# Optimization experiments

Hardware: AMD Instinct MI355X
Metric: run time of the kernel (lower is better)

## Reference

```python
import jax, jax.numpy as jnp
import numpy as np


def setup_inputs() -> dict:
    key = jax.random.key(0)
    k1, k2 = jax.random.split(key)
    x = jax.random.normal(k1, (4, 1, 16384), dtype=jnp.float32)  # [B, C, T]
    # dictionary initialized uniform(-1, 1) as in nn.Parameter(...).uniform_(-1, 1)
    d = jax.random.uniform(k2, (256, 1, 256), dtype=jnp.float32, minval=-1.0, maxval=1.0)  # [A, C, K]
    return {"x": x, "d": d, "n_iterations": 16}


def reference(x, d, n_iterations):
    B, C, T = x.shape
    A, _, K = d.shape
    pad = K // 2
    # normalize each atom over (channels, atom_size) dims, i.e. d_normalization_dims=(-1,-2)
    norms = jnp.linalg.norm(d.reshape(A, -1), axis=-1)
    dn = d / (norms[:, None, None] + 1e-12)

    # work in a padded domain so conv output position == start index in padded residual
    rp = jnp.pad(x, ((0, 0), (0, 0), (pad, pad)))        # residual, [B, C, T+2*pad]
    recon = jnp.zeros_like(rp)                            # accumulated reconstruction
    Tout = T + 2 * pad - K + 1                            # conv output length

    def step(carry, _):
        rp, recon = carry
        # cross-correlation of residual with every atom: [B, A, Tout]
        fm = jax.lax.conv_general_dilated(
            rp, dn, window_strides=(1,), padding='VALID',
            dimension_numbers=('NCH', 'OIH', 'NCH'))
        flat = fm.reshape(B, A * Tout)
        idx = jnp.argmax(flat, axis=-1)                   # signed max, per batch item
        val = jnp.take_along_axis(flat, idx[:, None], axis=-1)[:, 0]
        atom_idx = idx // Tout
        pos = idx % Tout                                  # start index in padded domain
        atoms = dn[atom_idx] * val[:, None, None]         # [B, C, K]

        def upd(r, rec, a, p):
            seg = jax.lax.dynamic_slice(r, (0, p), (C, K))
            r2 = jax.lax.dynamic_update_slice(r, seg - a, (0, p))
            segr = jax.lax.dynamic_slice(rec, (0, p), (C, K))
            rec2 = jax.lax.dynamic_update_slice(rec, segr + a, (0, p))
            return r2, rec2

        rp2, recon2 = jax.vmap(upd)(rp, recon, atoms, pos)
        return (rp2, recon2), None

    (rp, recon), _ = jax.lax.scan(step, (rp, recon), None, length=n_iterations)
    # crop padding -> reconstruction with same shape as x
    return recon[:, :, pad:pad + T]
```

## Files before the change

### kernel.cpp

```cpp
#include <hip/hip_runtime.h>
#include <math.h>

#define B    4
#define T    16384
#define A    256
#define K    256
#define PAD  128
#define TP   (T + 2*PAD)
#define TOUT (TP - K + 1)
#define ITERS 16
#define CHUNK 512
#define NCHUNK 33
#define NCP  36
#define TILE 2048
#define NTILE 9
#define NBLK 512
#define BPB2 128
#define HBASE 8192
#define RPSTORE 8448
#define RPN 8704
#define NGRP 8
#define SUBSTRIDE 32
#define BARSTRIDE (NGRP*SUBSTRIDE)
#define DLDS 40960

#define TAP(acc, s0,s1,s2,s3, dq) { acc = fmaf(s0,(dq).x,acc); acc = fmaf(s1,(dq).y,acc); \
                                    acc = fmaf(s2,(dq).z,acc); acc = fmaf(s3,(dq).w,acc); }

__device__ __forceinline__ void wave_amax(float& bv, int& bi) {
    #pragma unroll
    for (int off = 32; off; off >>= 1) {
        float ov = __shfl_down(bv, off);
        int   oi = __shfl_down(bi, off);
        if (ov > bv || (ov == bv && oi < bi)) { bv = ov; bi = oi; }
    }
}

struct KSmem {
    float  rp[RPN];
    float4 dn4[4][64];
    float  chv[4][34];
    int    chi[4][34];
    float  wv[16]; int wi[16];
    float  fv; int fi;
};

__device__ __forceinline__ void gbar_sub(unsigned* sub, int r, unsigned gen16, int tid,
                                         bool release_arrival, bool acquire_exit) {
    __syncthreads();
    if (tid == 0)
        __hip_atomic_fetch_add(&sub[(r >> 4)*SUBSTRIDE], 1u,
                               release_arrival ? __ATOMIC_RELEASE : __ATOMIC_RELAXED,
                               __HIP_MEMORY_SCOPE_AGENT);
    if (tid < 64) {
        for (;;) {
            unsigned ok = 1;
            if (tid < NGRP)
                ok = (__hip_atomic_load(&sub[tid*SUBSTRIDE], __ATOMIC_RELAXED,
                                        __HIP_MEMORY_SCOPE_AGENT) >= gen16);
            if (__all((int)ok)) break;
            __builtin_amdgcn_s_sleep(4);
        }
    }
    __syncthreads();
    if (acquire_exit) __builtin_amdgcn_fence(__ATOMIC_ACQUIRE, "agent");
}

__device__ void chunks_update(KSmem& sm, int baseF, int cA, int cB, int aBase, int tid) {
    const int lane = tid & 63, w = tid >> 6;
    const int grp = tid >> 7;
    const int cg = grp ? cB : cA;
    const int lt = cg*512 + (tid & 127)*4;
    float c0[4] = {0,0,0,0}, c1[4] = {0,0,0,0}, c2[4] = {0,0,0,0}, c3[4] = {0,0,0,0};
    if (cg >= 0) {
        const float4* srp4 = (const float4*)sm.rp;
        int ol4 = (lt - baseF) >> 2;
        float4 p = srp4[ol4];
        #pragma unroll 4
        for (int kq = 0; kq < 64; kq++) {
            float4 d0 = sm.dn4[0][kq];
            float4 d1 = sm.dn4[1][kq];
            float4 d2 = sm.dn4[2][kq];
            float4 d3 = sm.dn4[3][kq];
            float4 pn = srp4[ol4 + kq + 1];
            TAP(c0[0], p.x,p.y,p.z,p.w, d0); TAP(c0[1], p.y,p.z,p.w,pn.x, d0);
            TAP(c0[2], p.z,p.w,pn.x,pn.y, d0); TAP(c0[3], p.w,pn.x,pn.y,pn.z, d0);
            TAP(c1[0], p.x,p.y,p.z,p.w, d1); TAP(c1[1], p.y,p.z,p.w,pn.x, d1);
            TAP(c1[2], p.z,p.w,pn.x,pn.y, d1); TAP(c1[3], p.w,pn.x,pn.y,pn.z, d1);
            TAP(c2[0], p.x,p.y,p.z,p.w, d2); TAP(c2[1], p.y,p.z,p.w,pn.x, d2);
            TAP(c2[2], p.z,p.w,pn.x,pn.y, d2); TAP(c2[3], p.w,pn.x,pn.y,pn.z, d2);
            TAP(c3[0], p.x,p.y,p.z,p.w, d3); TAP(c3[1], p.y,p.z,p.w,pn.x, d3);
            TAP(c3[2], p.z,p.w,pn.x,pn.y, d3); TAP(c3[3], p.w,pn.x,pn.y,pn.z, d3);
            p = pn;
        }
    }
    float bv0 = -INFINITY, bv1 = -INFINITY, bv2 = -INFINITY, bv3 = -INFINITY;
    int bi0 = 0x7fffffff, bi1 = 0x7fffffff, bi2 = 0x7fffffff, bi3 = 0x7fffffff;
    if (cg >= 0) {
        #pragma unroll
        for (int j = 0; j < 4; j++) {
            int t = lt + j;
            if (t < TOUT) {
                if (c0[j] > bv0) { bv0 = c0[j]; bi0 = (aBase+0)*TOUT + t; }
                if (c1[j] > bv1) { bv1 = c1[j]; bi1 = (aBase+1)*TOUT + t; }
                if (c2[j] > bv2) { bv2 = c2[j]; bi2 = (aBase+2)*TOUT + t; }
                if (c3[j] > bv3) { bv3 = c3[j]; bi3 = (aBase+3)*TOUT + t; }
            }
        }
    }
    wave_amax(bv0, bi0); wave_amax(bv1, bi1); wave_amax(bv2, bi2); wave_amax(bv3, bi3);
    if (lane == 0) {
        sm.wv[0*4+w] = bv0; sm.wi[0*4+w] = bi0;
        sm.wv[1*4+w] = bv1; sm.wi[1*4+w] = bi1;
        sm.wv[2*4+w] = bv2; sm.wi[2*4+w] = bi2;
        sm.wv[3*4+w] = bv3; sm.wi[3*4+w] = bi3;
    }
    __syncthreads();
    if (tid < 8) {
        int a = tid >> 1, hh = tid & 1;
        int chunk = hh ? cB : cA;
        if (chunk >= 0) {
            float v0 = sm.wv[a*4 + 2*hh];   int i0 = sm.wi[a*4 + 2*hh];
            float v1 = sm.wv[a*4 + 2*hh+1]; int i1 = sm.wi[a*4 + 2*hh+1];
            if (v1 > v0 || (v1 == v0 && i1 < i0)) { v0 = v1; i0 = i1; }
            sm.chv[a][chunk] = v0; sm.chi[a][chunk] = i0;
        }
    }
    __syncthreads();
}

__device__ __forceinline__ void best_write1(KSmem& sm, int slot, int h, int tid,
                                            float* __restrict__ abv, int* __restrict__ abi) {
    const int lane = tid & 63, w = tid >> 6;
    int cstart = h ? 16 : 0, nch = h ? 17 : 16;
    float bv = -INFINITY; int bi = 0x7fffffff;
    if (lane < nch) { bv = sm.chv[w][cstart + lane]; bi = sm.chi[w][cstart + lane]; }
    wave_amax(bv, bi);
    if (lane == 0) { sm.wv[8+w] = bv; sm.wi[8+w] = bi; }
    __syncthreads();
    if (tid == 0) {
        float v = sm.wv[8]; int i = sm.wi[8];
        #pragma unroll
        for (int j = 1; j < 4; j++)
            if (sm.wv[8+j] > v || (sm.wv[8+j] == v && sm.wi[8+j] < i)) { v = sm.wv[8+j]; i = sm.wi[8+j]; }
        __hip_atomic_store(&abv[slot], v, __ATOMIC_RELAXED, __HIP_MEMORY_SCOPE_AGENT);
        __hip_atomic_store(&abi[slot], i, __ATOMIC_RELAXED, __HIP_MEMORY_SCOPE_AGENT);
    }
    asm volatile("s_waitcnt vmcnt(0)" ::: "memory");
}

__device__ __forceinline__ void pick1(KSmem& sm, int b, int tid,
                                      const float* __restrict__ avc, const int* __restrict__ aic) {
    const int lane = tid & 63, w = tid >> 6;
    float v = -INFINITY; int i = 0x7fffffff;
    if (tid < BPB2) {
        int s = b*BPB2 + tid;
        v = __hip_atomic_load(&avc[s], __ATOMIC_RELAXED, __HIP_MEMORY_SCOPE_AGENT);
        i = __hip_atomic_load(&aic[s], __ATOMIC_RELAXED, __HIP_MEMORY_SCOPE_AGENT);
    }
    if (w < 2) {
        wave_amax(v, i);
        if (lane == 0) { sm.wv[w] = v; sm.wi[w] = i; }
    }
    __syncthreads();
    if (tid == 0) {
        float bv = sm.wv[0]; int bi = sm.wi[0];
        if (sm.wv[1] > bv || (sm.wv[1] == bv && sm.wi[1] < bi)) { bv = sm.wv[1]; bi = sm.wi[1]; }
        sm.fv = bv; sm.fi = bi;
    }
    __syncthreads();
}

__global__ void __launch_bounds__(256, 2)
k_coop(const float* __restrict__ x, const float* __restrict__ d, float* __restrict__ out,
       float* __restrict__ dn,
       float* __restrict__ abv0, int* __restrict__ abi0,
       float* __restrict__ abv1, int* __restrict__ abi1, unsigned* __restrict__ bar) {
    extern __shared__ char raw[];
    KSmem& sm = *(KSmem*)raw;
    const int bid = blockIdx.x, tid = threadIdx.x;
    const int b = bid >> 7, r = bid & 127;
    const int h = r >> 6, a0 = r & 63;
    const int lane = tid & 63, w = tid >> 6;
    const int baseF = h * HBASE;
    const int cstart = h ? 16 : 0, cend = h ? 33 : 16;
    const int slot = b*BPB2 + r;
    unsigned* sub = bar + b*BARSTRIDE;

    {
        const float4* x4 = (const float4*)(x + (size_t)b*T);
        float4* rp4w = (float4*)sm.rp;
        int b4 = baseF >> 2;
        for (int i = tid; i < RPN/4; i += 256) {
            int g4 = b4 + i;
            float4 v = {0.f,0.f,0.f,0.f};
            if (i < RPSTORE/4 && g4 >= PAD/4 && g4 < (PAD+T)/4) v = x4[g4 - PAD/4];
            rp4w[i] = v;
        }
    }
    #pragma unroll
    for (int s = 0; s < 4; s++) {
        int atom = a0*4 + s;
        float v = d[atom*K + tid];
        float sq = v*v;
        #pragma unroll
        for (int off = 32; off; off >>= 1) sq += __shfl_down(sq, off);
        if (lane == 0) sm.wv[w] = sq;
        __syncthreads();
        float norm = sqrtf(sm.wv[0] + sm.wv[1] + sm.wv[2] + sm.wv[3]) + 1e-12f;
        float nv = v / norm;
        ((float*)&sm.dn4[s][0])[tid] = nv;
        dn[atom*K + tid] = nv;
        __syncthreads();
    }
    {
        int npass = h ? 9 : 8;
        for (int p = 0; p < npass; p++) {
            int ca = cstart + 2*p;
            int cb2 = (ca + 1 < cend) ? ca + 1 : -1;
            chunks_update(sm, baseF, ca, cb2, a0*4, tid);
        }
    }
    best_write1(sm, slot, h, tid, abv0, abi0);
    unsigned gen = 1;
    gbar_sub(sub, r, gen*16u, tid, true, true);

    const float* avc = abv0; const int* aic = abi0;
    float* avn = abv1; int* ain = abi1;
    for (int it = 0; it < ITERS-1; it++) {
        pick1(sm, b, tid, avc, aic);
        float val = sm.fv; int idx = sm.fi;
        int atom = idx / TOUT, pos = idx - atom*TOUT;
        float ds = dn[atom*K + tid];
        int li = pos + tid - baseF;
        if (li >= 0 && li < RPSTORE) sm.rp[li] -= val * ds;
        __syncthreads();
        int lo = pos - (K-1); if (lo < 0) lo = 0;
        int g0 = lo >> 9, g1 = g0 + 1;
        bool in0 = (g0 >= cstart && g0 < cend);
        bool in1 = (g1 >= cstart && g1 < cend);
        int ca = in0 ? g0 : (in1 ? g1 : -1);
        int cb2 = (in0 && in1) ? g1 : -1;
        if (ca >= 0) chunks_update(sm, baseF, ca, cb2, a0*4, tid);
        best_write1(sm, slot, h, tid, avn, ain);
        { const float* t1 = avc; avc = avn; avn = (float*)t1; }
        { const int*   t2 = aic; aic = ain; ain = (int*)t2; }
        gen++;
        gbar_sub(sub, r, gen*16u, tid, false, false);
    }
    if (a0 == 0) {
        pick1(sm, b, tid, avc, aic);
        float val = sm.fv; int idx = sm.fi;
        int atom = idx / TOUT, pos = idx - atom*TOUT;
        float ds = dn[atom*K + tid];
        int li = pos + tid - baseF;
        if (li >= 0 && li < RPSTORE) sm.rp[li] -= val * ds;
        __syncthreads();
        int o_lo4 = h ? (HBASE - PAD)/4 : 0;
        int o_hi4 = h ? T/4 : (HBASE - PAD)/4;
        const float4* xb4 = (const float4*)(x + (size_t)b*T);
        float4* o4 = (float4*)(out + (size_t)b*T);
        for (int i4 = o_lo4 + tid; i4 < o_hi4; i4 += 256) {
            float4 xv = xb4[i4];
            float4 rv = *(const float4*)&sm.rp[i4*4 + PAD - baseF];
            float4 ov; ov.x = xv.x - rv.x; ov.y = xv.y - rv.y;
            ov.z = xv.z - rv.z; ov.w = xv.w - rv.w;
            o4[i4] = ov;
        }
    }
}

struct Smem {
    float rp[TILE + K + 16];
    float dnA[K];
    float dnB[K];
    float dnsel[K];
    float wv[16]; int wi[16];
    float fv; int fi;
};

__device__ __forceinline__ void dev_norm(int a0, int tid, const float* __restrict__ d,
                                         float* __restrict__ dn, Smem& sm) {
    int lane = tid & 63, w = tid >> 6;
    #pragma unroll
    for (int s = 0; s < 2; s++) {
        int atom = a0*2 + s;
        float v = d[atom*K + tid];
        float sq = v*v;
        #pragma unroll
        for (int off = 32; off; off >>= 1) sq += __shfl_down(sq, off);
        if (lane == 0) sm.wv[w] = sq;
        __syncthreads();
        float norm = sqrtf(sm.wv[0] + sm.wv[1] + sm.wv[2] + sm.wv[3]) + 1e-12f;
        dn[atom*K + tid] = v / norm;
        __syncthreads();
    }
}

__device__ __forceinline__ void dev_init(int a0, int b, int tid, const float* __restrict__ x,
                                         float* __restrict__ rp, float* __restrict__ recon) {
    int i = a0*256 + tid;
    if (i < TP) {
        float v = (i >= PAD && i < PAD + T) ? x[b*T + (i - PAD)] : 0.f;
        rp[(size_t)b*TP + i] = v;
        recon[(size_t)b*TP + i] = 0.f;
    }
}

__device__ void dev_conv(int a0, int b, int tid, const float* __restrict__ rp,
                         const float* __restrict__ dn,
                         float* __restrict__ segval, int* __restrict__ segidx,
                         float* __restrict__ abv, int* __restrict__ abi, Smem& sm) {
    const int aA = a0*2, aB = a0*2 + 1;
    const int lane = tid & 63, w = tid >> 6;
    sm.dnA[tid] = dn[aA*K + tid];
    sm.dnB[tid] = dn[aB*K + tid];
    const float4* rp4 = (const float4*)(rp + (size_t)b*TP);

    for (int tile = 0; tile < NTILE; tile++) {
        int t0 = tile * TILE;
        __syncthreads();
        float4* s4 = (float4*)sm.rp;
        for (int i = tid; i < 580; i += 256) {
            int g = t0/4 + i;
            float4 v = {0.f,0.f,0.f,0.f};
            if (g*4 < TP) v = rp4[g];
            s4[i] = v;
        }
        __syncthreads();
        const float4* srp4 = (const float4*)sm.rp;
        const float4* dA4  = (const float4*)sm.dnA;
        const float4* dB4  = (const float4*)sm.dnB;
        float accA0[4] = {0,0,0,0}, accA1[4] = {0,0,0,0};
        float accB0[4] = {0,0,0,0}, accB1[4] = {0,0,0,0};
        float4 p = srp4[tid];
        float4 q = srp4[tid + 256];
        #pragma unroll 4
        for (int kq = 0; kq < 64; kq++) {
            float4 dA = dA4[kq];
            float4 dB = dB4[kq];
            float4 pn = srp4[tid + kq + 1];
            float4 qn = srp4[tid + 256 + kq + 1];
            TAP(accA0[0], p.x,p.y,p.z,p.w, dA); TAP(accA0[1], p.y,p.z,p.w,pn.x, dA);
            TAP(accA0[2], p.z,p.w,pn.x,pn.y, dA); TAP(accA0[3], p.w,pn.x,pn.y,pn.z, dA);
            TAP(accB0[0], p.x,p.y,p.z,p.w, dB); TAP(accB0[1], p.y,p.z,p.w,pn.x, dB);
            TAP(accB0[2], p.z,p.w,pn.x,pn.y, dB); TAP(accB0[3], p.w,pn.x,pn.y,pn.z, dB);
            TAP(accA1[0], q.x,q.y,q.z,q.w, dA); TAP(accA1[1], q.y,q.z,q.w,qn.x, dA);
            TAP(accA1[2], q.z,q.w,qn.x,qn.y, dA); TAP(accA1[3], q.w,qn.x,qn.y,qn.z, dA);
            TAP(accB1[0], q.x,q.y,q.z,q.w, dB); TAP(accB1[1], q.y,q.z,q.w,qn.x, dB);
            TAP(accB1[2], q.z,q.w,qn.x,qn.y, dB); TAP(accB1[3], q.w,qn.x,qn.y,qn.z, dB);
            p = pn; q = qn;
        }
        int lt = tid * 4;
        float bvA0 = -INFINITY, bvA1 = -INFINITY, bvB0 = -INFINITY, bvB1 = -INFINITY;
        int biA0 = 0x7fffffff, biA1 = 0x7fffffff, biB0 = 0x7fffffff, biB1 = 0x7fffffff;
        #pragma unroll
        for (int j = 0; j < 4; j++) {
            int t = t0 + lt + j;
            if (t < TOUT) {
                if (accA0[j] > bvA0) { bvA0 = accA0[j]; biA0 = aA*TOUT + t; }
                if (accB0[j] > bvB0) { bvB0 = accB0[j]; biB0 = aB*TOUT + t; }
            }
            int t1 = t0 + 1024 + lt + j;
            if (t1 < TOUT) {
                if (accA1[j] > bvA1) { bvA1 = accA1[j]; biA1 = aA*TOUT + t1; }
                if (accB1[j] > bvB1) { bvB1 = accB1[j]; biB1 = aB*TOUT + t1; }
            }
        }
        wave_amax(bvA0, biA0); wave_amax(bvA1, biA1);
        wave_amax(bvB0, biB0); wave_amax(bvB1, biB1);
        if (lane == 0) {
            sm.wv[w]    = bvA0; sm.wi[w]    = biA0;
            sm.wv[4+w]  = bvA1; sm.wi[4+w]  = biA1;
            sm.wv[8+w]  = bvB0; sm.wi[8+w]  = biB0;
            sm.wv[12+w] = bvB1; sm.wi[12+w] = biB1;
        }
        __syncthreads();
        if (tid < 4) {
            float v0 = sm.wv[2*tid];   int i0 = sm.wi[2*tid];
            float v1 = sm.wv[2*tid+1]; int i1 = sm.wi[2*tid+1];
            if (v1 > v0 || (v1 == v0 && i1 < i0)) { v0 = v1; i0 = i1; }
            int chunk = tile*4 + tid;
            if (chunk < NCHUNK) {
                segval[((size_t)b*A + aA)*NCP + chunk] = v0;
                segidx[((size_t)b*A + aA)*NCP + chunk] = i0;
            }
        } else if (tid >= 64 && tid < 68) {
            int c = tid - 64;
            float v0 = sm.wv[8+2*c];   int i0 = sm.wi[8+2*c];
            float v1 = sm.wv[8+2*c+1]; int i1 = sm.wi[8+2*c+1];
            if (v1 > v0 || (v1 == v0 && i1 < i0)) { v0 = v1; i0 = i1; }
            int chunk = tile*4 + c;
            if (chunk < NCHUNK) {
                segval[((size_t)b*A + aB)*NCP + chunk] = v0;
                segidx[((size_t)b*A + aB)*NCP + chunk] = i0;
            }
        }
    }
    __syncthreads();
    if (w < 2) {
        int atom = (w == 0) ? aA : aB;
        float bv = -INFINITY; int bi = 0x7fffffff;
        if (lane < NCHUNK) {
            bv = segval[((size_t)b*A + atom)*NCP + lane];
            bi = segidx[((size_t)b*A + atom)*NCP + lane];
        }
        wave_amax(bv, bi);
        if (lane == 0) { abv[b*A + atom] = bv; abi[b*A + atom] = bi; }
    }
}

__device__ void dev_iter(int a0, int b, int tid, int last,
                         const float* __restrict__ avc, const int* __restrict__ aic,
                         float* __restrict__ avn, int* __restrict__ ain,
                         const float* __restrict__ rin, float* __restrict__ rout,
                         float* __restrict__ recon, const float* __restrict__ dn,
                         float* __restrict__ segval, int* __restrict__ segidx, Smem& sm) {
    const int aA = a0*2, aB = a0*2 + 1;
    const int lane = tid & 63, w = tid >> 6;

    float bv0 = avc[b*A + tid]; int bi0 = aic[b*A + tid];
    const float4* rin4 = (const float4*)(rin + (size_t)b*TP);
    const int icopy = a0*256 + tid;
    const bool docopy = (!last) && (icopy < TP/4);
    float4 vcopy = {0.f,0.f,0.f,0.f};
    if (docopy) vcopy = rin4[icopy];
    sm.dnA[tid] = dn[aA*K + tid];
    sm.dnB[tid] = dn[aB*K + tid];

    {
        float bv = bv0; int bi = bi0;
        wave_amax(bv, bi);
        if (lane == 0) { sm.wv[w] = bv; sm.wi[w] = bi; }
        __syncthreads();
        if (tid == 0) {
            bv = sm.wv[0]; bi = sm.wi[0];
            for (int j = 1; j < 4; j++)
                if (sm.wv[j] > bv || (sm.wv[j] == bv && sm.wi[j] < bi)) { bv = sm.wv[j]; bi = sm.wi[j]; }
            sm.fv = bv; sm.fi = bi;
        }
        __syncthreads();
    }
    float val = sm.fv; int idx = sm.fi;
    int atom = idx / TOUT, pos = idx - atom*TOUT;
    sm.dnsel[tid] = dn[atom*K + tid];

    int lo = pos - (K-1); if (lo < 0) lo = 0;
    int c_lo = lo >> 9;
    int tbase = c_lo * CHUNK;

    if (!last) {
        float4* s4 = (float4*)sm.rp;
        for (int i = tid; i < 324; i += 256) {
            int g = tbase/4 + i;
            float4 v = {0.f,0.f,0.f,0.f};
            if (g*4 < TP) v = rin4[g];
            s4[i] = v;
        }
    }
    __syncthreads();
    if (docopy) {
        float4* rout4 = (float4*)(rout + (size_t)b*TP);
        float4 v = vcopy;
        int o = icopy*4 - pos;
        if (o > -4 && o < K) {
            if (o+0 >= 0 && o+0 < K) v.x -= val * sm.dnsel[o+0];
            if (o+1 >= 0 && o+1 < K) v.y -= val * sm.dnsel[o+1];
            if (o+2 >= 0 && o+2 < K) v.z -= val * sm.dnsel[o+2];
            if (o+3 >= 0 && o+3 < K) v.w -= val * sm.dnsel[o+3];
        }
        rout4[icopy] = v;
    }
    if (a0 == 0) {
        recon[(size_t)b*TP + pos + tid] += val * sm.dnsel[tid];
    }
    if (last) return;

    sm.rp[pos + tid - tbase] -= val * sm.dnsel[tid];
    __syncthreads();

    const float4* srp4 = (const float4*)sm.rp;
    const float4* dA4  = (const float4*)sm.dnA;
    const float4* dB4  = (const float4*)sm.dnB;
    float cA[4] = {0,0,0,0}, cB[4] = {0,0,0,0};
    float4 p = srp4[tid];
    #pragma unroll 4
    for (int kq = 0; kq < 64; kq++) {
        float4 dA = dA4[kq];
        float4 dB = dB4[kq];
        float4 pn = srp4[tid + kq + 1];
        TAP(cA[0], p.x,p.y,p.z,p.w, dA); TAP(cA[1], p.y,p.z,p.w,pn.x, dA);
        TAP(cA[2], p.z,p.w,pn.x,pn.y, dA); TAP(cA[3], p.w,pn.x,pn.y,pn.z, dA);
        TAP(cB[0], p.x,p.y,p.z,p.w, dB); TAP(cB[1], p.y,p.z,p.w,pn.x, dB);
        TAP(cB[2], p.z,p.w,pn.x,pn.y, dB); TAP(cB[3], p.w,pn.x,pn.y,pn.z, dB);
        p = pn;
    }
    int lt = tid * 4;
    float bvA = -INFINITY, bvB = -INFINITY;
    int biA = 0x7fffffff, biB = 0x7fffffff;
    #pragma unroll
    for (int j = 0; j < 4; j++) {
        int t = tbase + lt + j;
        if (t < TOUT) {
            if (cA[j] > bvA) { bvA = cA[j]; biA = aA*TOUT + t; }
            if (cB[j] > bvB) { bvB = cB[j]; biB = aB*TOUT + t; }
        }
    }
    wave_amax(bvA, biA); wave_amax(bvB, biB);
    if (lane == 0) { sm.wv[w] = bvA; sm.wi[w] = biA; sm.wv[8+w] = bvB; sm.wi[8+w] = biB; }
    __syncthreads();
    if (tid < 2) {
        float v0 = sm.wv[2*tid];   int i0 = sm.wi[2*tid];
        float v1 = sm.wv[2*tid+1]; int i1 = sm.wi[2*tid+1];
        if (v1 > v0 || (v1 == v0 && i1 < i0)) { v0 = v1; i0 = i1; }
        int chunk = c_lo + tid;
        if (chunk < NCHUNK) {
            segval[((size_t)b*A + aA)*NCP + chunk] = v0;
            segidx[((size_t)b*A + aA)*NCP + chunk] = i0;
        }
    } else if (tid >= 64 && tid < 66) {
        int c = tid - 64;
        float v0 = sm.wv[8+2*c];   int i0 = sm.wi[8+2*c];
        float v1 = sm.wv[8+2*c+1]; int i1 = sm.wi[8+2*c+1];
        if (v1 > v0 || (v1 == v0 && i1 < i0)) { v0 = v1; i0 = i1; }
        int chunk = c_lo + c;
        if (chunk < NCHUNK) {
            segval[((size_t)b*A + aB)*NCP + chunk] = v0;
            segidx[((size_t)b*A + aB)*NCP + chunk] = i0;
        }
    }
    __syncthreads();
    if (w < 2) {
        int at = (w == 0) ? aA : aB;
        float bv = -INFINITY; int bi = 0x7fffffff;
        if (lane < NCHUNK) {
            bv = segval[((size_t)b*A + at)*NCP + lane];
            bi = segidx[((size_t)b*A + at)*NCP + lane];
        }
        wave_amax(bv, bi);
        if (lane == 0) { avn[b*A + at] = bv; ain[b*A + at] = bi; }
    }
}

__global__ void __launch_bounds__(256) k_f_norm_init(const float* x, const float* d,
                                                     float* dn, float* rp0, float* recon) {
    __shared__ Smem sm;
    dev_norm(blockIdx.x & 127, threadIdx.x, d, dn, sm);
    dev_init(blockIdx.x & 127, blockIdx.x >> 7, threadIdx.x, x, rp0, recon);
}
__global__ void __launch_bounds__(256, 2) k_f_conv(const float* rp, const float* dn,
                                                   float* segval, int* segidx,
                                                   float* abv, int* abi) {
    __shared__ Smem sm;
    dev_conv(blockIdx.x & 127, blockIdx.x >> 7, threadIdx.x, rp, dn, segval, segidx, abv, abi, sm);
}
__global__ void __launch_bounds__(256, 2) k_f_iter(int last,
                                                   const float* avc, const int* aic,
                                                   float* avn, int* ain,
                                                   const float* rin, float* rout,
                                                   float* recon, const float* dn,
                                                   float* segval, int* segidx) {
    __shared__ Smem sm;
    dev_iter(blockIdx.x & 127, blockIdx.x >> 7, threadIdx.x, last,
             avc, aic, avn, ain, rin, rout, recon, dn, segval, segidx, sm);
}
__global__ void k_f_out(const float* recon, float* out) {
    int i = blockIdx.x * blockDim.x + threadIdx.x;
    if (i >= B*T) return;
    int b = i / T, t = i - b*T;
    out[i] = recon[(size_t)b*TP + PAD + t];
}

extern "C" void kernel_launch(void* const* d_in, const int* in_sizes, int n_in,
                              void* d_out, int out_size, void* d_ws, size_t ws_size,
                              hipStream_t stream) {
    const float* x = (const float*)d_in[0];
    const float* d = (const float*)d_in[1];
    float* out = (float*)d_out;

    float* ws     = (float*)d_ws;
    float* dn     = ws;
    float* rp0    = dn  + (size_t)A*K;
    float* rp1    = rp0 + (size_t)B*TP;
    float* recon  = rp1 + (size_t)B*TP;
    float* segval = recon + (size_t)B*TP;
    int*   segidx = (int*)(segval + (size_t)B*A*NCP);
    float* abv0   = (float*)(segidx + (size_t)B*A*NCP);
    float* abv1   = abv0 + (size_t)B*2*A;
    int*   abi0   = (int*)(abv1 + (size_t)B*2*A);
    int*   abi1   = abi0 + (size_t)B*2*A;
    unsigned* bar = (unsigned*)(abi1 + (size_t)B*2*A);

    (void)hipFuncSetAttribute((const void*)k_coop,
                              hipFuncAttributeMaxDynamicSharedMemorySize, DLDS);
    int nb = 0, ncu = 0;
    hipError_t e1 = hipOccupancyMaxActiveBlocksPerMultiprocessor(&nb, (const void*)k_coop,
                                                                 256, DLDS);
    hipError_t e2 = hipDeviceGetAttribute(&ncu, hipDeviceAttributeMultiprocessorCount, 0);
    bool coop = (e1 == hipSuccess && e2 == hipSuccess && nb > 0 && ncu > 0 &&
                 (long)nb * ncu >= NBLK);
    if (coop) {
        (void)hipMemsetAsync(bar, 0, B*BARSTRIDE*sizeof(unsigned), stream);
        hipLaunchKernelGGL(k_coop, dim3(NBLK), dim3(256), DLDS, stream,
                           x, d, out, dn, abv0, abi0, abv1, abi1, bar);
        return;
    }
    k_f_norm_init<<<NBLK, 256, 0, stream>>>(x, d, dn, rp0, recon);
    k_f_conv<<<NBLK, 256, 0, stream>>>(rp0, dn, segval, segidx, abv0, abi0);
    float* rbuf[2] = {rp0, rp1};
    float* av[2]   = {abv0, abv1};
    int*   ai[2]   = {abi0, abi1};
    for (int it = 0; it < ITERS; it++) {
        k_f_iter<<<NBLK, 256, 0, stream>>>(it == ITERS-1 ? 1 : 0,
                                           av[it & 1], ai[it & 1],
                                           av[(it + 1) & 1], ai[(it + 1) & 1],
                                           rbuf[it & 1], rbuf[(it + 1) & 1],
                                           recon, dn, segval, segidx);
    }
    k_f_out<<<(B*T + 255)/256, 256, 0, stream>>>(recon, out);
}
```

Baseline: 522.1 us.

## Replace per-iteration grid barrier with generation-tagged packed slot polling

Drops the global sub-barrier that ran after every matching-pursuit iteration. Each block now publishes its best (value, index) as one 64-bit word tagged with a generation number. Readers spin on each slot until the expected generation appears. The two-buffer alternation keeps a slot from being overwritten before all readers of the previous generation have consumed it. This removes the cost of a barrier round trip per iteration, at the cost of per-slot polling traffic and packing the index into 23 bits.

```diff
diff --git a/kernel.cpp b/kernel.cpp
--- a/kernel.cpp
+++ b/kernel.cpp
@@ -27,6 +27,8 @@
 #define TAP(acc, s0,s1,s2,s3, dq) { acc = fmaf(s0,(dq).x,acc); acc = fmaf(s1,(dq).y,acc); \
                                     acc = fmaf(s2,(dq).z,acc); acc = fmaf(s3,(dq).w,acc); }
 
+typedef unsigned long long u64;
+
 __device__ __forceinline__ void wave_amax(float& bv, int& bi) {
     #pragma unroll
     for (int off = 32; off; off >>= 1) {
@@ -45,13 +47,11 @@
     float  fv; int fi;
 };
 
-__device__ __forceinline__ void gbar_sub(unsigned* sub, int r, unsigned gen16, int tid,
-                                         bool release_arrival, bool acquire_exit) {
+__device__ __forceinline__ void gbar_sub(unsigned* sub, int r, unsigned gen16, int tid) {
     __syncthreads();
     if (tid == 0)
         __hip_atomic_fetch_add(&sub[(r >> 4)*SUBSTRIDE], 1u,
-                               release_arrival ? __ATOMIC_RELEASE : __ATOMIC_RELAXED,
-                               __HIP_MEMORY_SCOPE_AGENT);
+                               __ATOMIC_RELEASE, __HIP_MEMORY_SCOPE_AGENT);
     if (tid < 64) {
         for (;;) {
             unsigned ok = 1;
@@ -63,7 +63,7 @@
         }
     }
     __syncthreads();
-    if (acquire_exit) __builtin_amdgcn_fence(__ATOMIC_ACQUIRE, "agent");
+    __builtin_amdgcn_fence(__ATOMIC_ACQUIRE, "agent");
 }
 
 __device__ void chunks_update(KSmem& sm, int baseF, int cA, int cB, int aBase, int tid) {
@@ -129,8 +129,7 @@
     __syncthreads();
 }
 
-__device__ __forceinline__ void best_write1(KSmem& sm, int slot, int h, int tid,
-                                            float* __restrict__ abv, int* __restrict__ abi) {
+__device__ __forceinline__ void slot_write(KSmem& sm, u64* wp, int gen, int h, int tid) {
     const int lane = tid & 63, w = tid >> 6;
     int cstart = h ? 16 : 0, nch = h ? 17 : 16;
     float bv = -INFINITY; int bi = 0x7fffffff;
@@ -143,20 +142,26 @@
         #pragma unroll
         for (int j = 1; j < 4; j++)
             if (sm.wv[8+j] > v || (sm.wv[8+j] == v && sm.wi[8+j] < i)) { v = sm.wv[8+j]; i = sm.wi[8+j]; }
-        __hip_atomic_store(&abv[slot], v, __ATOMIC_RELAXED, __HIP_MEMORY_SCOPE_AGENT);
-        __hip_atomic_store(&abi[slot], i, __ATOMIC_RELAXED, __HIP_MEMORY_SCOPE_AGENT);
-    }
-    asm volatile("s_waitcnt vmcnt(0)" ::: "memory");
-}
-
-__device__ __forceinline__ void pick1(KSmem& sm, int b, int tid,
-                                      const float* __restrict__ avc, const int* __restrict__ aic) {
+        u64 e = ((u64)(unsigned)(gen + 1) << 56)
+              | ((u64)__float_as_uint(v) << 24)
+              | (u64)(unsigned)i;
+        __hip_atomic_store(wp, e, __ATOMIC_RELAXED, __HIP_MEMORY_SCOPE_AGENT);
+    }
+}
+
+__device__ __forceinline__ void pick_poll(KSmem& sm, const u64* sl, int gen, int tid) {
     const int lane = tid & 63, w = tid >> 6;
     float v = -INFINITY; int i = 0x7fffffff;
     if (tid < BPB2) {
-        int s = b*BPB2 + tid;
-        v = __hip_atomic_load(&avc[s], __ATOMIC_RELAXED, __HIP_MEMORY_SCOPE_AGENT);
-        i = __hip_atomic_load(&aic[s], __ATOMIC_RELAXED, __HIP_MEMORY_SCOPE_AGENT);
+        const u64* p = sl + tid;
+        u64 e;
+        for (;;) {
+            e = __hip_atomic_load(p, __ATOMIC_RELAXED, __HIP_MEMORY_SCOPE_AGENT);
+            if ((unsigned)(e >> 56) == (unsigned)(gen + 1)) break;
+            __builtin_amdgcn_s_sleep(1);
+        }
+        v = __uint_as_float((unsigned)((e >> 24) & 0xFFFFFFFFull));
+        i = (int)(e & 0x7FFFFF);
     }
     if (w < 2) {
         wave_amax(v, i);
@@ -173,9 +178,7 @@
 
 __global__ void __launch_bounds__(256, 2)
 k_coop(const float* __restrict__ x, const float* __restrict__ d, float* __restrict__ out,
-       float* __restrict__ dn,
-       float* __restrict__ abv0, int* __restrict__ abi0,
-       float* __restrict__ abv1, int* __restrict__ abi1, unsigned* __restrict__ bar) {
+       float* __restrict__ dn, u64* __restrict__ slots, unsigned* __restrict__ bar) {
     extern __shared__ char raw[];
     KSmem& sm = *(KSmem*)raw;
     const int bid = blockIdx.x, tid = threadIdx.x;
@@ -184,7 +187,7 @@
     const int lane = tid & 63, w = tid >> 6;
     const int baseF = h * HBASE;
     const int cstart = h ? 16 : 0, cend = h ? 33 : 16;
-    const int slot = b*BPB2 + r;
+    u64* slotsb = slots + (size_t)b*2*BPB2;
     unsigned* sub = bar + b*BARSTRIDE;
 
     {
@@ -221,14 +224,11 @@
             chunks_update(sm, baseF, ca, cb2, a0*4, tid);
         }
     }
-    best_write1(sm, slot, h, tid, abv0, abi0);
-    unsigned gen = 1;
-    gbar_sub(sub, r, gen*16u, tid, true, true);
-
-    const float* avc = abv0; const int* aic = abi0;
-    float* avn = abv1; int* ain = abi1;
+    slot_write(sm, slotsb + 0*BPB2 + r, 0, h, tid);
+    gbar_sub(sub, r, 16u, tid);
+
     for (int it = 0; it < ITERS-1; it++) {
-        pick1(sm, b, tid, avc, aic);
+        pick_poll(sm, slotsb + (it & 1)*BPB2, it, tid);
         float val = sm.fv; int idx = sm.fi;
         int atom = idx / TOUT, pos = idx - atom*TOUT;
         float ds = dn[atom*K + tid];
@@ -242,14 +242,10 @@
         int ca = in0 ? g0 : (in1 ? g1 : -1);
         int cb2 = (in0 && in1) ? g1 : -1;
         if (ca >= 0) chunks_update(sm, baseF, ca, cb2, a0*4, tid);
-        best_write1(sm, slot, h, tid, avn, ain);
-        { const float* t1 = avc; avc = avn; avn = (float*)t1; }
-        { const int*   t2 = aic; aic = ain; ain = (int*)t2; }
-        gen++;
-        gbar_sub(sub, r, gen*16u, tid, false, false);
+        slot_write(sm, slotsb + ((it+1) & 1)*BPB2 + r, it+1, h, tid);
     }
     if (a0 == 0) {
-        pick1(sm, b, tid, avc, aic);
+        pick_poll(sm, slotsb + ((ITERS-1) & 1)*BPB2, ITERS-1, tid);
         float val = sm.fv; int idx = sm.fi;
         int atom = idx / TOUT, pos = idx - atom*TOUT;
         float ds = dn[atom*K + tid];
@@ -590,6 +586,7 @@
     int*   abi0   = (int*)(abv1 + (size_t)B*2*A);
     int*   abi1   = abi0 + (size_t)B*2*A;
     unsigned* bar = (unsigned*)(abi1 + (size_t)B*2*A);
+    u64*  slots   = (u64*)(bar + (size_t)B*BARSTRIDE);
 
     (void)hipFuncSetAttribute((const void*)k_coop,
                               hipFuncAttributeMaxDynamicSharedMemorySize, DLDS);
@@ -601,8 +598,9 @@
                  (long)nb * ncu >= NBLK);
     if (coop) {
         (void)hipMemsetAsync(bar, 0, B*BARSTRIDE*sizeof(unsigned), stream);
+        (void)hipMemsetAsync(slots, 0xFF, (size_t)B*2*BPB2*sizeof(u64), stream);
         hipLaunchKernelGGL(k_coop, dim3(NBLK), dim3(256), DLDS, stream,
-                           x, d, out, dn, abv0, abi0, abv1, abi1, bar);
+                           x, d, out, dn, slots, bar);
         return;
     }
     k_f_norm_init<<<NBLK, 256, 0, stream>>>(x, d, dn, rp0, recon);
```

Result: no change. 517.0 us (-1.0%).
